# Optimization experiments

Measured on AMD Instinct MI355X. Metric: run time of the kernel, lower is better.

Reference implementation:

```python
import jax, jax.numpy as jnp
import numpy as np

N = 8192      # num nodes
D = 256       # input feature dim (num_embeddings)
F_OUT = 128   # out_channels
B = 4096      # lookup batch size


def setup_inputs() -> dict:
    key = jax.random.key(0)
    k1, k2, k3, k4 = jax.random.split(key, 4)
    x = jax.random.randint(k1, (B,), 0, N)                      # node ids for final lookup
    adj = jax.random.randint(k2, (N, N), 0, 2).astype(jnp.int32)  # dense 0/1 adjacency
    embedding = jax.random.normal(k3, (N, D), dtype=jnp.float32)
    xavier = 1.414 * (6.0 / (D + F_OUT)) ** 0.5
    W = jax.random.uniform(k4, (D, F_OUT), minval=-xavier, maxval=xavier, dtype=jnp.float32)
    return {"x": x, "adj": adj, "embedding": embedding, "W": W}


def reference(x, adj, embedding, W):
    Wh = embedding @ W                                   # [N, F_OUT]
    mask = adj > 0
    maskf = mask.astype(Wh.dtype)
    # per-row neighbor mean of Wh (vectorized form of the python row loop)
    deg = jnp.maximum(jnp.sum(maskf, axis=1), 1.0)       # guard; random adj has deg>0
    neigh_mean = (maskf @ Wh) / deg[:, None]             # [N, F_OUT]
    alpha = jnp.sum(Wh * neigh_mean, axis=1)             # [N], Wh[i] . mean(neighbors)
    e = Wh @ Wh.T + alpha[:, None]                       # similarity + row-wise query term
    att = jax.nn.softmax(jnp.where(mask, e, jnp.asarray(-9e15, e.dtype)), axis=1)
    # dropout is identity in eval mode (p effectively 0)
    h_prime = att @ Wh                                   # [N, F_OUT]
    emb_out = jax.nn.elu(h_prime)                        # concat=True branch
    out = emb_out[x]                                     # F.embedding lookup, [B, F_OUT]
    nrm = jnp.linalg.norm(out, axis=1, keepdims=True)
    return out / jnp.maximum(nrm, 1e-12)                 # F.normalize (L2, eps=1e-12)
```

## Files before the change

### kernel.cpp

```cpp
#include <hip/hip_runtime.h>

#define NN 8192
#define DD 256
#define FF 128
#define BB 4096
#define NSPLIT 8
#define KCHUNK (NN / NSPLIT)

typedef unsigned short ushortT;
typedef __attribute__((ext_vector_type(8))) short bf16x8;
typedef __attribute__((ext_vector_type(4))) float f32x4;

__device__ __forceinline__ ushortT f2bf(float f) {
  unsigned u = __float_as_uint(f);
  return (ushortT)((u + 0x7FFFu + ((u >> 16) & 1u)) >> 16);
}
__device__ __forceinline__ float bf2f(ushortT h) {
  return __uint_as_float(((unsigned)h) << 16);
}


__global__ __launch_bounds__(256) void init_kernel(int* flags, int* cnt) {
  int i = blockIdx.x * 256 + threadIdx.x;
  flags[i] = 0;
  if (i == 0) *cnt = 0;
}

__global__ __launch_bounds__(256) void scatter_kernel(const int* __restrict__ x, int* flags) {
  int b = blockIdx.x * 256 + threadIdx.x;
  flags[x[b]] = 1;
}

__global__ __launch_bounds__(256) void compact_kernel(const int* __restrict__ flags, int* cnt,
                                                      int* list, int* slot) {
  int i = blockIdx.x * 256 + threadIdx.x;
  if (flags[i]) {
    int pos = atomicAdd(cnt, 1);
    list[pos] = i;
    slot[i] = pos;
  }
}


__global__ __launch_bounds__(256) void wh_kernel(const float* __restrict__ emb,
                                                 const float* __restrict__ W,
                                                 ushortT* __restrict__ Whh,
                                                 ushortT* __restrict__ Whl) {
  __shared__ float Es[32 * 65];
  __shared__ float Ws[64 * 128];
  const int t = threadIdx.x;
  const int r0 = blockIdx.x * 32;
  const int rg = t >> 5;
  const int cg = t & 31;
  float4 acc[4] = {{0,0,0,0},{0,0,0,0},{0,0,0,0},{0,0,0,0}};
  for (int kc = 0; kc < DD; kc += 64) {
    __syncthreads();
    for (int i = 0; i < 8; ++i) {
      int idx = t + 256 * i;
      int r = idx >> 6, k = idx & 63;
      Es[r * 65 + k] = emb[(r0 + r) * DD + kc + k];
    }
    for (int i = 0; i < 8; ++i) {
      int idx = t + 256 * i;
      int kr = idx >> 5, c4 = (idx & 31) * 4;
      *(float4*)&Ws[kr * 128 + c4] = *(const float4*)&W[(kc + kr) * 128 + c4];
    }
    __syncthreads();
    for (int k = 0; k < 64; ++k) {
      float4 b = *(const float4*)&Ws[k * 128 + cg * 4];
#pragma unroll
      for (int i = 0; i < 4; ++i) {
        float a = Es[(rg * 4 + i) * 65 + k];
        acc[i].x += a * b.x; acc[i].y += a * b.y;
        acc[i].z += a * b.z; acc[i].w += a * b.w;
      }
    }
  }
#pragma unroll
  for (int i = 0; i < 4; ++i) {
    int row = r0 + rg * 4 + i;
    float v[4] = {acc[i].x, acc[i].y, acc[i].z, acc[i].w};
    ushort4 hh, ll;
    ushortT* hp = (ushortT*)&hh;
    ushortT* lp = (ushortT*)&ll;
#pragma unroll
    for (int k = 0; k < 4; ++k) {
      ushortT h = f2bf(v[k]);
      hp[k] = h;
      lp[k] = f2bf(v[k] - bf2f(h));
    }
    *(ushort4*)&Whh[row * FF + cg * 4] = hh;
    *(ushort4*)&Whl[row * FF + cg * 4] = ll;
  }
}


__global__ __launch_bounds__(256) void transpose_kernel(const ushortT* __restrict__ A,
                                                        ushortT* __restrict__ At) {
  __shared__ ushortT tile[128 * 136];
  const int t = threadIdx.x;
  const int r0 = blockIdx.x * 128;
  for (int i = 0; i < 8; ++i) {
    int idx = t + 256 * i;
    int r = idx >> 4, c8 = idx & 15;
    *(bf16x8*)&tile[r * 136 + c8 * 8] = *(const bf16x8*)&A[(r0 + r) * FF + c8 * 8];
  }
  __syncthreads();
  for (int i = 0; i < 8; ++i) {
    int idx = t + 256 * i;
    int f = idx >> 4, r8 = idx & 15;
    bf16x8 v;
#pragma unroll
    for (int u = 0; u < 8; ++u) v[u] = (short)tile[(r8 * 8 + u) * 136 + f];
    *(bf16x8*)&At[(size_t)f * NN + r0 + r8 * 8] = v;
  }
}


__global__ __launch_bounds__(64) void attn_kernel(
    const ushortT* __restrict__ Whh, const ushortT* __restrict__ Whl,
    const ushortT* __restrict__ WhT, const int* __restrict__ adj,
    const int* __restrict__ list, const int* __restrict__ cntp,
    float* __restrict__ Opart, float* __restrict__ mpart, float* __restrict__ lpart) {
  __shared__ short Ps[16 * 72];
  const int cnt = *cntp;
  const int qt = blockIdx.x >> 3;
  const int chunk = blockIdx.x & 7;
  const int q0 = qt * 16;
  if (q0 >= cnt) return;

  const int l = threadIdx.x;
  const int quad = l >> 4, c = l & 15;

  const int qidc = list[min(q0 + c, cnt - 1)];
  const ushortT* qph = Whh + (size_t)qidc * FF + quad * 8;
  const ushortT* qpl = Whl + (size_t)qidc * FF + quad * 8;
  bf16x8 qh[4], ql[4];
#pragma unroll
  for (int ks = 0; ks < 4; ++ks) {
    qh[ks] = *(const bf16x8*)(qph + ks * 32);
    ql[ks] = *(const bf16x8*)(qpl + ks * 32);
  }
  size_t arow[4];
#pragma unroll
  for (int r = 0; r < 4; ++r)
    arow[r] = (size_t)list[min(q0 + quad * 4 + r, cnt - 1)] * NN;

  float m[4], lr[4];
#pragma unroll
  for (int r = 0; r < 4; ++r) { m[r] = -1e30f; lr[r] = 0.f; }
  f32x4 O[8] = {{0,0,0,0},{0,0,0,0},{0,0,0,0},{0,0,0,0},
                {0,0,0,0},{0,0,0,0},{0,0,0,0},{0,0,0,0}};

  const int kt0 = chunk * KCHUNK;
  for (int kt = kt0; kt < kt0 + KCHUNK; kt += 64) {
    int av[4][4];
#pragma unroll
    for (int nt = 0; nt < 4; ++nt)
#pragma unroll
      for (int r = 0; r < 4; ++r) av[nt][r] = adj[arow[r] + kt + nt * 16 + c];

    f32x4 sacc[4];
#pragma unroll
    for (int nt = 0; nt < 4; ++nt) {
      const ushortT* kh = Whh + (size_t)(kt + nt * 16 + c) * FF + quad * 8;
      const ushortT* kl = Whl + (size_t)(kt + nt * 16 + c) * FF + quad * 8;
      f32x4 a = {0, 0, 0, 0};
#pragma unroll
      for (int ks = 0; ks < 4; ++ks) {
        bf16x8 bh = *(const bf16x8*)(kh + ks * 32);
        bf16x8 bl = *(const bf16x8*)(kl + ks * 32);
        a = __builtin_amdgcn_mfma_f32_16x16x32_bf16(qh[ks], bh, a, 0, 0, 0);
        a = __builtin_amdgcn_mfma_f32_16x16x32_bf16(ql[ks], bh, a, 0, 0, 0);
        a = __builtin_amdgcn_mfma_f32_16x16x32_bf16(qh[ks], bl, a, 0, 0, 0);
      }
      sacc[nt] = a;
    }

    float rmax[4];
#pragma unroll
    for (int r = 0; r < 4; ++r) {
      float v = -1e30f;
#pragma unroll
      for (int nt = 0; nt < 4; ++nt) v = fmaxf(v, av[nt][r] > 0 ? sacc[nt][r] : -1e30f);
      rmax[r] = v;
    }
#pragma unroll
    for (int mk = 1; mk <= 8; mk <<= 1)
#pragma unroll
      for (int r = 0; r < 4; ++r) rmax[r] = fmaxf(rmax[r], __shfl_xor(rmax[r], mk, 16));
    float sc[4], psum[4];
#pragma unroll
    for (int r = 0; r < 4; ++r) {
      float nm = fmaxf(m[r], rmax[r]);
      sc[r] = __expf(m[r] - nm);
      m[r] = nm;
      psum[r] = 0.f;
    }
#pragma unroll
    for (int nt = 0; nt < 4; ++nt)
#pragma unroll
      for (int r = 0; r < 4; ++r) {
        float p = av[nt][r] > 0 ? __expf(sacc[nt][r] - m[r]) : 0.f;
        ushortT pb = f2bf(p);
        Ps[(quad * 4 + r) * 72 + nt * 16 + c] = (short)pb;
        psum[r] += bf2f(pb);
      }
#pragma unroll
    for (int mk = 1; mk <= 8; mk <<= 1)
#pragma unroll
      for (int r = 0; r < 4; ++r) psum[r] += __shfl_xor(psum[r], mk, 16);
#pragma unroll
    for (int r = 0; r < 4; ++r) lr[r] = lr[r] * sc[r] + psum[r];

#pragma unroll
    for (int ft = 0; ft < 8; ++ft)
#pragma unroll
      for (int r = 0; r < 4; ++r) O[ft][r] *= sc[r];
    bf16x8 pa[2];
#pragma unroll
    for (int ks2 = 0; ks2 < 2; ++ks2)
      pa[ks2] = *(const bf16x8*)&Ps[c * 72 + ks2 * 32 + quad * 8];
#pragma unroll
    for (int ft = 0; ft < 8; ++ft) {
      const ushortT* vp = WhT + (size_t)(ft * 16 + c) * NN + kt + quad * 8;
#pragma unroll
      for (int ks2 = 0; ks2 < 2; ++ks2) {
        bf16x8 vb = *(const bf16x8*)(vp + ks2 * 32);
        O[ft] = __builtin_amdgcn_mfma_f32_16x16x32_bf16(pa[ks2], vb, O[ft], 0, 0, 0);
      }
    }
  }

  float* Op = Opart + (size_t)chunk * 4096 * FF;
#pragma unroll
  for (int ft = 0; ft < 8; ++ft)
#pragma unroll
    for (int r = 0; r < 4; ++r)
      Op[(size_t)(q0 + quad * 4 + r) * FF + ft * 16 + c] = O[ft][r];
  if (c == 0) {
#pragma unroll
    for (int r = 0; r < 4; ++r) {
      mpart[chunk * 4096 + q0 + quad * 4 + r] = m[r];
      lpart[chunk * 4096 + q0 + quad * 4 + r] = lr[r];
    }
  }
}


__global__ __launch_bounds__(128) void combine_kernel(
    const float* __restrict__ Opart, const float* __restrict__ mpart,
    const float* __restrict__ lpart, float* __restrict__ h) {
  const int r = blockIdx.x;
  const int t = threadIdx.x;
  float mstar = -1e30f;
#pragma unroll
  for (int c = 0; c < NSPLIT; ++c) mstar = fmaxf(mstar, mpart[c * 4096 + r]);
  float lstar = 0.f, acc = 0.f;
#pragma unroll
  for (int c = 0; c < NSPLIT; ++c) {
    float wgt = __expf(mpart[c * 4096 + r] - mstar);
    lstar += wgt * lpart[c * 4096 + r];
    acc += wgt * Opart[((size_t)c * 4096 + r) * FF + t];
  }
  float v = acc / fmaxf(lstar, 1e-30f);
  h[r * FF + t] = v > 0.f ? v : expm1f(v);
}


__global__ __launch_bounds__(128) void out_kernel(const int* __restrict__ x,
                                                  const int* __restrict__ slot,
                                                  const float* __restrict__ h,
                                                  float* __restrict__ out) {
  const int b = blockIdx.x, t = threadIdx.x;
  const int s = slot[x[b]];
  float v = h[s * FF + t];
  float ss = v * v;
#pragma unroll
  for (int wd = 1; wd <= 32; wd <<= 1) ss += __shfl_xor(ss, wd);
  __shared__ float red[2];
  if ((t & 63) == 0) red[t >> 6] = ss;
  __syncthreads();
  float tot = red[0] + red[1];
  float scale = 1.f / fmaxf(sqrtf(tot), 1e-12f);
  out[b * FF + t] = v * scale;
}


extern "C" void kernel_launch(void* const* d_in, const int* in_sizes, int n_in,
                              void* d_out, int out_size, void* d_ws, size_t ws_size,
                              hipStream_t stream) {
  const int*   x   = (const int*)d_in[0];
  const int*   adj = (const int*)d_in[1];
  const float* emb = (const float*)d_in[2];
  const float* W   = (const float*)d_in[3];
  float* out = (float*)d_out;

  char* base = (char*)d_ws;
  ushortT* Whh = (ushortT*)(base);
  ushortT* Whl = (ushortT*)(base + 2097152);
  float*   h   = (float*)(base + 2097152);
  ushortT* WhT = (ushortT*)(base + 4194304);
  float* Opart = (float*)(base + 6291456);
  float* mpart = (float*)(base + 23068672);
  float* lpart = (float*)(base + 23199744);
  int*   flags = (int*)(base + 23330816);
  int*   list  = (int*)(base + 23363584);
  int*   slot  = (int*)(base + 23379968);
  int*   cnt   = (int*)(base + 23412736);
  (void)in_sizes; (void)n_in; (void)out_size; (void)ws_size;

  hipLaunchKernelGGL(init_kernel,      dim3(NN / 256), dim3(256), 0, stream, flags, cnt);
  hipLaunchKernelGGL(scatter_kernel,   dim3(BB / 256), dim3(256), 0, stream, x, flags);
  hipLaunchKernelGGL(compact_kernel,   dim3(NN / 256), dim3(256), 0, stream, flags, cnt, list, slot);
  hipLaunchKernelGGL(wh_kernel,        dim3(NN / 32),  dim3(256), 0, stream, emb, W, Whh, Whl);
  hipLaunchKernelGGL(transpose_kernel, dim3(NN / 128), dim3(256), 0, stream, Whh, WhT);
  hipLaunchKernelGGL(attn_kernel,      dim3((BB / 16) * NSPLIT), dim3(64), 0, stream,
                     Whh, Whl, WhT, adj, list, cnt, Opart, mpart, lpart);
  hipLaunchKernelGGL(combine_kernel,   dim3(4096), dim3(128), 0, stream, Opart, mpart, lpart, h);
  hipLaunchKernelGGL(out_kernel,       dim3(BB),   dim3(128), 0, stream, x, slot, h, out);
}
```

Measured before the change: 514.1 us.

## Bit-pack adjacency rows and share double-buffered LDS key tiles across four waves

```diff
diff --git a/kernel.cpp b/kernel.cpp
--- a/kernel.cpp
+++ b/kernel.cpp
@@ -6,6 +6,7 @@
 #define BB 4096
 #define NSPLIT 8
 #define KCHUNK (NN / NSPLIT)
+#define NITER (KCHUNK / 64)
 
 typedef unsigned short ushortT;
 typedef __attribute__((ext_vector_type(8))) short bf16x8;
@@ -38,6 +39,24 @@
     int pos = atomicAdd(cnt, 1);
     list[pos] = i;
     slot[i] = pos;
+  }
+}
+
+
+__global__ __launch_bounds__(256) void pack_kernel(const int* __restrict__ adj,
+                                                   const int* __restrict__ list,
+                                                   const int* __restrict__ cntp,
+                                                   unsigned* __restrict__ pk) {
+  const int s = blockIdx.x >> 2;
+  const int kc = (blockIdx.x & 3) * 2048;
+  if (s >= *cntp) return;
+  const int w = threadIdx.x >> 6, l = threadIdx.x & 63;
+  const int* base = adj + (size_t)list[s] * NN + kc + w * 512;
+  unsigned long long* dst = (unsigned long long*)(pk + s * 256 + (kc >> 5) + w * 16);
+#pragma unroll
+  for (int i = 0; i < 8; ++i) {
+    unsigned long long b = __ballot(base[i * 64 + l] > 0);
+    if (l == 0) dst[i] = b;
   }
 }
 
@@ -97,54 +116,63 @@
 
 __global__ __launch_bounds__(256) void transpose_kernel(const ushortT* __restrict__ A,
                                                         ushortT* __restrict__ At) {
-  __shared__ ushortT tile[128 * 136];
+  __shared__ ushortT tile[64 * 72];
   const int t = threadIdx.x;
-  const int r0 = blockIdx.x * 128;
-  for (int i = 0; i < 8; ++i) {
+  const int r0 = (blockIdx.x >> 1) * 64, c0 = (blockIdx.x & 1) * 64;
+#pragma unroll
+  for (int i = 0; i < 2; ++i) {
     int idx = t + 256 * i;
-    int r = idx >> 4, c8 = idx & 15;
-    *(bf16x8*)&tile[r * 136 + c8 * 8] = *(const bf16x8*)&A[(r0 + r) * FF + c8 * 8];
+    int r = idx >> 3, cb = idx & 7;
+    *(bf16x8*)&tile[r * 72 + ((cb ^ ((r >> 3) & 7)) * 8)] =
+        *(const bf16x8*)&A[(size_t)(r0 + r) * FF + c0 + cb * 8];
   }
   __syncthreads();
-  for (int i = 0; i < 8; ++i) {
+#pragma unroll
+  for (int i = 0; i < 2; ++i) {
     int idx = t + 256 * i;
-    int f = idx >> 4, r8 = idx & 15;
+    int f = idx >> 3, r8 = idx & 7;
     bf16x8 v;
 #pragma unroll
-    for (int u = 0; u < 8; ++u) v[u] = (short)tile[(r8 * 8 + u) * 136 + f];
-    *(bf16x8*)&At[(size_t)f * NN + r0 + r8 * 8] = v;
-  }
-}
-
-
-__global__ __launch_bounds__(64) void attn_kernel(
+    for (int u = 0; u < 8; ++u) {
+      int row = r8 * 8 + u;
+      v[u] = (short)tile[row * 72 + (((f >> 3) ^ ((row >> 3) & 7)) * 8) + (f & 7)];
+    }
+    *(bf16x8*)&At[(size_t)(c0 + f) * NN + r0 + r8 * 8] = v;
+  }
+}
+
+
+__global__ __launch_bounds__(256) void attn_kernel(
     const ushortT* __restrict__ Whh, const ushortT* __restrict__ Whl,
-    const ushortT* __restrict__ WhT, const int* __restrict__ adj,
+    const ushortT* __restrict__ WhT, const unsigned* __restrict__ pk,
     const int* __restrict__ list, const int* __restrict__ cntp,
     float* __restrict__ Opart, float* __restrict__ mpart, float* __restrict__ lpart) {
-  __shared__ short Ps[16 * 72];
+  __shared__ short Kh[2][64 * 128];
+  __shared__ short Kl[2][64 * 128];
+  __shared__ short Ps[4][16 * 72];
+  __shared__ int nid[64];
+
   const int cnt = *cntp;
-  const int qt = blockIdx.x >> 3;
-  const int chunk = blockIdx.x & 7;
-  const int q0 = qt * 16;
+  const int qblk = blockIdx.x >> 3, chunk = blockIdx.x & 7;
+  const int q0 = qblk * 64;
   if (q0 >= cnt) return;
 
-  const int l = threadIdx.x;
-  const int quad = l >> 4, c = l & 15;
-
-  const int qidc = list[min(q0 + c, cnt - 1)];
-  const ushortT* qph = Whh + (size_t)qidc * FF + quad * 8;
-  const ushortT* qpl = Whl + (size_t)qidc * FF + quad * 8;
+  const int t = threadIdx.x;
+  if (t < 64) nid[t] = list[min(q0 + t, cnt - 1)];
+  __syncthreads();
+
+  const int w = t >> 6, l = t & 63, quad = l >> 4, c = l & 15;
+
+  const size_t qr = (size_t)nid[w * 16 + c] * FF;
   bf16x8 qh[4], ql[4];
 #pragma unroll
   for (int ks = 0; ks < 4; ++ks) {
-    qh[ks] = *(const bf16x8*)(qph + ks * 32);
-    ql[ks] = *(const bf16x8*)(qpl + ks * 32);
-  }
-  size_t arow[4];
-#pragma unroll
-  for (int r = 0; r < 4; ++r)
-    arow[r] = (size_t)list[min(q0 + quad * 4 + r, cnt - 1)] * NN;
+    qh[ks] = *(const bf16x8*)(Whh + qr + ks * 32 + quad * 8);
+    ql[ks] = *(const bf16x8*)(Whl + qr + ks * 32 + quad * 8);
+  }
+  int prow[4];
+#pragma unroll
+  for (int r = 0; r < 4; ++r) prow[r] = min(q0 + w * 16 + quad * 4 + r, cnt - 1);
 
   float m[4], lr[4];
 #pragma unroll
@@ -153,23 +181,58 @@
                 {0,0,0,0},{0,0,0,0},{0,0,0,0},{0,0,0,0}};
 
   const int kt0 = chunk * KCHUNK;
-  for (int kt = kt0; kt < kt0 + KCHUNK; kt += 64) {
-    int av[4][4];
-#pragma unroll
-    for (int nt = 0; nt < 4; ++nt)
-#pragma unroll
-      for (int r = 0; r < 4; ++r) av[nt][r] = adj[arow[r] + kt + nt * 16 + c];
+
+  bf16x8 sgh[4], sgl[4];
+  {
+    const ushortT* gh = Whh + (size_t)kt0 * FF;
+    const ushortT* gl = Whl + (size_t)kt0 * FF;
+#pragma unroll
+    for (int i = 0; i < 4; ++i) {
+      int idx = t + 256 * i;
+      sgh[i] = *(const bf16x8*)(gh + idx * 8);
+      sgl[i] = *(const bf16x8*)(gl + idx * 8);
+    }
+#pragma unroll
+    for (int i = 0; i < 4; ++i) {
+      int idx = t + 256 * i;
+      int r = idx >> 4, cb = idx & 15;
+      int off = r * 128 + ((cb ^ (r & 7)) * 8);
+      *(bf16x8*)&Kh[0][off] = sgh[i];
+      *(bf16x8*)&Kl[0][off] = sgl[i];
+    }
+  }
+
+  for (int it = 0; it < NITER; ++it) {
+    const int kt = kt0 + it * 64;
+    const int cur = it & 1;
+    if (it + 1 < NITER) {
+      const ushortT* gh = Whh + (size_t)(kt + 64) * FF;
+      const ushortT* gl = Whl + (size_t)(kt + 64) * FF;
+#pragma unroll
+      for (int i = 0; i < 4; ++i) {
+        int idx = t + 256 * i;
+        sgh[i] = *(const bf16x8*)(gh + idx * 8);
+        sgl[i] = *(const bf16x8*)(gl + idx * 8);
+      }
+    }
+    unsigned mw0[4], mw1[4];
+#pragma unroll
+    for (int r = 0; r < 4; ++r) {
+      uint2 mm = *(const uint2*)(pk + (size_t)prow[r] * 256 + (kt >> 5));
+      mw0[r] = mm.x; mw1[r] = mm.y;
+    }
+    __syncthreads();
 
     f32x4 sacc[4];
 #pragma unroll
     for (int nt = 0; nt < 4; ++nt) {
-      const ushortT* kh = Whh + (size_t)(kt + nt * 16 + c) * FF + quad * 8;
-      const ushortT* kl = Whl + (size_t)(kt + nt * 16 + c) * FF + quad * 8;
+      const int rb = (nt * 16 + c) * 128;
       f32x4 a = {0, 0, 0, 0};
 #pragma unroll
       for (int ks = 0; ks < 4; ++ks) {
-        bf16x8 bh = *(const bf16x8*)(kh + ks * 32);
-        bf16x8 bl = *(const bf16x8*)(kl + ks * 32);
+        const int off = rb + (((ks * 4 + quad) ^ (c & 7)) * 8);
+        bf16x8 bh = *(const bf16x8*)&Kh[cur][off];
+        bf16x8 bl = *(const bf16x8*)&Kl[cur][off];
         a = __builtin_amdgcn_mfma_f32_16x16x32_bf16(qh[ks], bh, a, 0, 0, 0);
         a = __builtin_amdgcn_mfma_f32_16x16x32_bf16(ql[ks], bh, a, 0, 0, 0);
         a = __builtin_amdgcn_mfma_f32_16x16x32_bf16(qh[ks], bl, a, 0, 0, 0);
@@ -182,7 +245,10 @@
     for (int r = 0; r < 4; ++r) {
       float v = -1e30f;
 #pragma unroll
-      for (int nt = 0; nt < 4; ++nt) v = fmaxf(v, av[nt][r] > 0 ? sacc[nt][r] : -1e30f);
+      for (int nt = 0; nt < 4; ++nt) {
+        unsigned bit = ((nt < 2 ? mw0[r] : mw1[r]) >> ((nt & 1) * 16 + c)) & 1u;
+        v = fmaxf(v, bit ? sacc[nt][r] : -1e30f);
+      }
       rmax[r] = v;
     }
 #pragma unroll
@@ -201,9 +267,10 @@
     for (int nt = 0; nt < 4; ++nt)
 #pragma unroll
       for (int r = 0; r < 4; ++r) {
-        float p = av[nt][r] > 0 ? __expf(sacc[nt][r] - m[r]) : 0.f;
+        unsigned bit = ((nt < 2 ? mw0[r] : mw1[r]) >> ((nt & 1) * 16 + c)) & 1u;
+        float p = bit ? __expf(sacc[nt][r] - m[r]) : 0.f;
         ushortT pb = f2bf(p);
-        Ps[(quad * 4 + r) * 72 + nt * 16 + c] = (short)pb;
+        Ps[w][(quad * 4 + r) * 72 + nt * 16 + c] = (short)pb;
         psum[r] += bf2f(pb);
       }
 #pragma unroll
@@ -220,7 +287,7 @@
     bf16x8 pa[2];
 #pragma unroll
     for (int ks2 = 0; ks2 < 2; ++ks2)
-      pa[ks2] = *(const bf16x8*)&Ps[c * 72 + ks2 * 32 + quad * 8];
+      pa[ks2] = *(const bf16x8*)&Ps[w][c * 72 + ks2 * 32 + quad * 8];
 #pragma unroll
     for (int ft = 0; ft < 8; ++ft) {
       const ushortT* vp = WhT + (size_t)(ft * 16 + c) * NN + kt + quad * 8;
@@ -230,6 +297,17 @@
         O[ft] = __builtin_amdgcn_mfma_f32_16x16x32_bf16(pa[ks2], vb, O[ft], 0, 0, 0);
       }
     }
+
+    if (it + 1 < NITER) {
+#pragma unroll
+      for (int i = 0; i < 4; ++i) {
+        int idx = t + 256 * i;
+        int r = idx >> 4, cb = idx & 15;
+        int off = r * 128 + ((cb ^ (r & 7)) * 8);
+        *(bf16x8*)&Kh[1 - cur][off] = sgh[i];
+        *(bf16x8*)&Kl[1 - cur][off] = sgl[i];
+      }
+    }
   }
 
   float* Op = Opart + (size_t)chunk * 4096 * FF;
@@ -237,12 +315,12 @@
   for (int ft = 0; ft < 8; ++ft)
 #pragma unroll
     for (int r = 0; r < 4; ++r)
-      Op[(size_t)(q0 + quad * 4 + r) * FF + ft * 16 + c] = O[ft][r];
+      Op[(size_t)(q0 + w * 16 + quad * 4 + r) * FF + ft * 16 + c] = O[ft][r];
   if (c == 0) {
 #pragma unroll
     for (int r = 0; r < 4; ++r) {
-      mpart[chunk * 4096 + q0 + quad * 4 + r] = m[r];
-      lpart[chunk * 4096 + q0 + quad * 4 + r] = lr[r];
+      mpart[chunk * 4096 + q0 + w * 16 + quad * 4 + r] = m[r];
+      lpart[chunk * 4096 + q0 + w * 16 + quad * 4 + r] = lr[r];
     }
   }
 }
@@ -304,19 +382,21 @@
   float* Opart = (float*)(base + 6291456);
   float* mpart = (float*)(base + 23068672);
   float* lpart = (float*)(base + 23199744);
-  int*   flags = (int*)(base + 23330816);
-  int*   list  = (int*)(base + 23363584);
-  int*   slot  = (int*)(base + 23379968);
-  int*   cnt   = (int*)(base + 23412736);
+  unsigned* pk = (unsigned*)(base + 23330816);
+  int*   flags = (int*)(base + 27525120);
+  int*   list  = (int*)(base + 27557888);
+  int*   slot  = (int*)(base + 27574272);
+  int*   cnt   = (int*)(base + 27607040);
   (void)in_sizes; (void)n_in; (void)out_size; (void)ws_size;
 
   hipLaunchKernelGGL(init_kernel,      dim3(NN / 256), dim3(256), 0, stream, flags, cnt);
   hipLaunchKernelGGL(scatter_kernel,   dim3(BB / 256), dim3(256), 0, stream, x, flags);
   hipLaunchKernelGGL(compact_kernel,   dim3(NN / 256), dim3(256), 0, stream, flags, cnt, list, slot);
+  hipLaunchKernelGGL(pack_kernel,      dim3(4096 * 4), dim3(256), 0, stream, adj, list, cnt, pk);
   hipLaunchKernelGGL(wh_kernel,        dim3(NN / 32),  dim3(256), 0, stream, emb, W, Whh, Whl);
-  hipLaunchKernelGGL(transpose_kernel, dim3(NN / 128), dim3(256), 0, stream, Whh, WhT);
-  hipLaunchKernelGGL(attn_kernel,      dim3((BB / 16) * NSPLIT), dim3(64), 0, stream,
-                     Whh, Whl, WhT, adj, list, cnt, Opart, mpart, lpart);
+  hipLaunchKernelGGL(transpose_kernel, dim3((NN / 64) * 2), dim3(256), 0, stream, Whh, WhT);
+  hipLaunchKernelGGL(attn_kernel,      dim3((BB / 64) * NSPLIT), dim3(256), 0, stream,
+                     Whh, Whl, WhT, pk, list, cnt, Opart, mpart, lpart);
   hipLaunchKernelGGL(combine_kernel,   dim3(4096), dim3(128), 0, stream, Opart, mpart, lpart, h);
   hipLaunchKernelGGL(out_kernel,       dim3(BB),   dim3(128), 0, stream, x, slot, h, out);
 }
```

After: 463.8 us. 9.8% less time.
